# Performance work log

Measured on AMD Instinct MI355X. Metric: run time of the kernel, lower is better.

The kernel has to match this reference:

```python
import jax, jax.numpy as jnp
import numpy as np

IN_FEATURES = 4096
OUT_FEATURES = 14336
TOPK_RATIO = 0.3
TOPK = int(IN_FEATURES * TOPK_RATIO)  # 1228


def setup_inputs() -> dict:
    key = jax.random.key(0)
    k1, k2, k3 = jax.random.split(key, 3)
    x = jax.random.normal(k1, (1, 1, IN_FEATURES), dtype=jnp.float32)
    weight = jax.random.normal(k2, (OUT_FEATURES, IN_FEATURES), dtype=jnp.float32)
    bias = jax.random.normal(k3, (OUT_FEATURES,), dtype=jnp.float32)
    return {"x": x, "weight": weight, "bias": bias}


def reference(x, weight, bias):
    # Decode path (bsz*seq == 1), first-call cache miss: indices come from
    # the current activation's top-k |x| values (recall==1.0 branch).
    bsz, seq, _ = x.shape
    xf = x.reshape(-1)  # [in_features]
    # argsort(|x|, descending)[:topk] == top_k on |x| (tie order irrelevant for the math)
    _, idx = jax.lax.top_k(jnp.abs(xf).astype(jnp.float32), TOPK)  # [topk]
    x_slice = xf[idx]                 # [topk]
    w_slice = weight[:, idx]          # [out_features, topk]
    # x[:, indices] @ weight_slice.T + bias
    out = jnp.einsum("k,ok->o", x_slice, w_slice) + bias  # [out_features]
    return out.reshape(bsz, seq, OUT_FEATURES)
```

## Files before the change

### kernel.cpp

```cpp
#include <hip/hip_runtime.h>
#include <hip/hip_bf16.h>

#define N_IN 4096
#define N_OUT 14336
#define TOPK 1228

__global__ __launch_bounds__(1024) void topk_mask_kernel(
    const float* __restrict__ x, float* __restrict__ x_masked) {
  __shared__ unsigned int s_abs[N_IN];
  __shared__ unsigned int s_hist[256];
  __shared__ unsigned int s_pk[4];
  __shared__ unsigned long long s_cmask[N_IN / 64];
  __shared__ unsigned int s_cbase[N_IN / 64];

  const int tid = threadIdx.x;
  const int lane = tid & 63;

#pragma unroll
  for (int it = 0; it < N_IN / 1024; ++it) {
    const int i = it * 1024 + tid;
    s_abs[i] = __float_as_uint(x[i]) & 0x7fffffffu;
  }
  if (tid == 0) { s_pk[0] = 0u; s_pk[1] = TOPK; }
  __syncthreads();

  for (int pass = 3; pass >= 0; --pass) {
    const unsigned int prefix = s_pk[0];
    const unsigned int krem = s_pk[1];
    if (tid < 256) s_hist[tid] = 0u;
    __syncthreads();

    const int shift = pass * 8;
    const unsigned int maskAbove =
        (pass == 3) ? 0u : (0xFFFFFFFFu << (shift + 8));

#pragma unroll
    for (int it = 0; it < N_IN / 1024; ++it) {
      const int i = it * 1024 + tid;
      const unsigned int b = s_abs[i];
      const bool active = ((b & maskAbove) == prefix);
      const unsigned int bucket = (b >> shift) & 0xFFu;
      unsigned long long m = __ballot(active);
#pragma unroll
      for (int bit = 0; bit < 8; ++bit) {
        const unsigned long long vote =
            __ballot(active && ((bucket >> bit) & 1u));
        m &= ((bucket >> bit) & 1u) ? vote : ~vote;
      }
      if (active) {
        const int leader = __ffsll((unsigned long long)m) - 1;
        if (lane == leader)
          atomicAdd(&s_hist[bucket], (unsigned int)__popcll(m));
      }
    }
    __syncthreads();

    if (tid < 64) {
      const unsigned int h0 = s_hist[tid * 4 + 0];
      const unsigned int h1 = s_hist[tid * 4 + 1];
      const unsigned int h2 = s_hist[tid * 4 + 2];
      const unsigned int h3 = s_hist[tid * 4 + 3];
      const unsigned int s = h0 + h1 + h2 + h3;
      unsigned int inc = s;
#pragma unroll
      for (int off = 1; off < 64; off <<= 1) {
        const unsigned int v = __shfl_down(inc, off, 64);
        if (tid + off < 64) inc += v;
      }
      const unsigned int U = inc - s;
      const unsigned int C3 = U + h3;
      const unsigned int C2 = C3 + h2;
      const unsigned int C1 = C2 + h1;
      const unsigned int C0 = C1 + h0;
      const unsigned int Carr[4] = {C0, C1, C2, C3};
      const unsigned int Sarr[4] = {C1, C2, C3, U};
      const unsigned int hv[4] = {h0, h1, h2, h3};
#pragma unroll
      for (int j = 0; j < 4; ++j) {
        if (Sarr[j] < krem && krem <= Carr[j]) {
          s_pk[0] = prefix | ((unsigned int)(tid * 4 + j) << shift);
          s_pk[1] = krem - Sarr[j];
          s_pk[2] = hv[j];
        }
      }
    }
    __syncthreads();
  }

  const unsigned int t_abs = s_pk[0];
  const unsigned int need = s_pk[1];
  const unsigned int eqc = s_pk[2];

  if (eqc == need) {
#pragma unroll
    for (int it = 0; it < N_IN / 1024; ++it) {
      const int i = it * 1024 + tid;
      x_masked[i] = (s_abs[i] >= t_abs) ? x[i] : 0.0f;
    }
  } else {
#pragma unroll
    for (int it = 0; it < N_IN / 1024; ++it) {
      const int i = it * 1024 + tid;
      const bool eq = (s_abs[i] == t_abs);
      const unsigned long long m = __ballot(eq);
      if (lane == 0) s_cmask[i >> 6] = m;
    }
    __syncthreads();
    if (tid < 64) {
      const unsigned int cnt = (unsigned int)__popcll(s_cmask[tid]);
      unsigned int inc = cnt;
#pragma unroll
      for (int off = 1; off < 64; off <<= 1) {
        const unsigned int v = __shfl_up(inc, off, 64);
        if (lane >= off) inc += v;
      }
      s_cbase[tid] = inc - cnt;
    }
    __syncthreads();
#pragma unroll
    for (int it = 0; it < N_IN / 1024; ++it) {
      const int i = it * 1024 + tid;
      const unsigned int b = s_abs[i];
      bool sel = (b > t_abs);
      if (b == t_abs) {
        const unsigned long long below =
            s_cmask[i >> 6] & ((1ull << lane) - 1ull);
        sel = (s_cbase[i >> 6] + (unsigned int)__popcll(below)) < need;
      }
      x_masked[i] = sel ? x[i] : 0.0f;
    }
  }
}

__global__ __launch_bounds__(256) void masked_matvec_kernel(
    const float* __restrict__ xm, const float* __restrict__ W,
    const float* __restrict__ bias, float* __restrict__ out) {
  __shared__ __align__(16) float s_x[N_IN];

  const int tid = threadIdx.x;
  for (int i = tid; i < N_IN; i += 256) s_x[i] = xm[i];
  __syncthreads();

  const int wave = tid >> 6;
  const int lane = tid & 63;
  const int row = blockIdx.x * 4 + wave;
  const float4* __restrict__ wr4 =
      reinterpret_cast<const float4*>(W + (size_t)row * N_IN);
  const float4* s_x4 = reinterpret_cast<const float4*>(s_x);

  float a0 = 0.0f, a1 = 0.0f, a2 = 0.0f, a3 = 0.0f;
#pragma unroll
  for (int it = 0; it < 4; ++it) {
    const int b = it * 4 * 64 + lane;
    const float4 w0 = wr4[b + 0 * 64];
    const float4 w1 = wr4[b + 1 * 64];
    const float4 w2 = wr4[b + 2 * 64];
    const float4 w3 = wr4[b + 3 * 64];
    const float4 v0 = s_x4[b + 0 * 64];
    const float4 v1 = s_x4[b + 1 * 64];
    const float4 v2 = s_x4[b + 2 * 64];
    const float4 v3 = s_x4[b + 3 * 64];
    a0 += w0.x * v0.x + w0.y * v0.y + w0.z * v0.z + w0.w * v0.w;
    a1 += w1.x * v1.x + w1.y * v1.y + w1.z * v1.z + w1.w * v1.w;
    a2 += w2.x * v2.x + w2.y * v2.y + w2.z * v2.z + w2.w * v2.w;
    a3 += w3.x * v3.x + w3.y * v3.y + w3.z * v3.z + w3.w * v3.w;
  }
  float acc = (a0 + a1) + (a2 + a3);

#pragma unroll
  for (int off = 32; off >= 1; off >>= 1) acc += __shfl_down(acc, off, 64);

  if (lane == 0) out[row] = acc + bias[row];
}

extern "C" void kernel_launch(void* const* d_in, const int* in_sizes, int n_in,
                              void* d_out, int out_size, void* d_ws,
                              size_t ws_size, hipStream_t stream) {
  const float* x    = (const float*)d_in[0];
  const float* W    = (const float*)d_in[1];
  const float* bias = (const float*)d_in[2];
  float* out = (float*)d_out;
  float* xm  = (float*)d_ws;

  topk_mask_kernel<<<1, 1024, 0, stream>>>(x, xm);
  masked_matvec_kernel<<<N_OUT / 4, 256, 0, stream>>>(xm, W, bias, out);
}
```

Measured before the change: 54.84 us.

## Process two rows per wave, read x from global, stagger column phase

The matvec kernel now has each wave compute two output rows, so each block covers 8 rows. It drops the LDS staging of x and keeps the whole x slice for each lane in registers, loaded straight from global memory (L2-cached). Column chunks are visited in a rotating order offset per row pair, which spreads concurrent loads across memory channels. The cost is heavier register use (16 float4 of x plus weight prefetch), which may lower occupancy on a kernel bound by memory bandwidth.

```diff
diff --git a/kernel.cpp b/kernel.cpp
--- a/kernel.cpp
+++ b/kernel.cpp
@@ -135,42 +135,67 @@
 __global__ __launch_bounds__(256) void masked_matvec_kernel(
     const float* __restrict__ xm, const float* __restrict__ W,
     const float* __restrict__ bias, float* __restrict__ out) {
-  __shared__ __align__(16) float s_x[N_IN];
-
   const int tid = threadIdx.x;
-  for (int i = tid; i < N_IN; i += 256) s_x[i] = xm[i];
-  __syncthreads();
-
   const int wave = tid >> 6;
   const int lane = tid & 63;
-  const int row = blockIdx.x * 4 + wave;
-  const float4* __restrict__ wr4 =
-      reinterpret_cast<const float4*>(W + (size_t)row * N_IN);
-  const float4* s_x4 = reinterpret_cast<const float4*>(s_x);
-
-  float a0 = 0.0f, a1 = 0.0f, a2 = 0.0f, a3 = 0.0f;
-#pragma unroll
-  for (int it = 0; it < 4; ++it) {
-    const int b = it * 4 * 64 + lane;
-    const float4 w0 = wr4[b + 0 * 64];
-    const float4 w1 = wr4[b + 1 * 64];
-    const float4 w2 = wr4[b + 2 * 64];
-    const float4 w3 = wr4[b + 3 * 64];
-    const float4 v0 = s_x4[b + 0 * 64];
-    const float4 v1 = s_x4[b + 1 * 64];
-    const float4 v2 = s_x4[b + 2 * 64];
-    const float4 v3 = s_x4[b + 3 * 64];
-    a0 += w0.x * v0.x + w0.y * v0.y + w0.z * v0.z + w0.w * v0.w;
-    a1 += w1.x * v1.x + w1.y * v1.y + w1.z * v1.z + w1.w * v1.w;
-    a2 += w2.x * v2.x + w2.y * v2.y + w2.z * v2.z + w2.w * v2.w;
-    a3 += w3.x * v3.x + w3.y * v3.y + w3.z * v3.z + w3.w * v3.w;
-  }
-  float acc = (a0 + a1) + (a2 + a3);
-
-#pragma unroll
-  for (int off = 32; off >= 1; off >>= 1) acc += __shfl_down(acc, off, 64);
-
-  if (lane == 0) out[row] = acc + bias[row];
+  const int r0 = blockIdx.x * 8 + wave * 2;
+  const int phase = (r0 >> 1) & 15;
+
+  const float4* __restrict__ w0r4 =
+      reinterpret_cast<const float4*>(W + (size_t)r0 * N_IN);
+  const float4* __restrict__ w1r4 =
+      reinterpret_cast<const float4*>(W + (size_t)(r0 + 1) * N_IN);
+  const float4* __restrict__ x4 = reinterpret_cast<const float4*>(xm);
+
+  float4 p0[4], p1[4];
+#pragma unroll
+  for (int j = 0; j < 4; ++j) {
+    const int c = (phase + j) & 15;
+    p0[j] = w0r4[c * 64 + lane];
+    p1[j] = w1r4[c * 64 + lane];
+  }
+
+  float4 xv[16];
+#pragma unroll
+  for (int j = 0; j < 16; ++j) {
+    const int c = (phase + j) & 15;
+    xv[j] = x4[c * 64 + lane];
+  }
+
+  float a0[4], a1[4];
+#pragma unroll
+  for (int j = 0; j < 4; ++j) {
+    a0[j] = p0[j].x * xv[j].x + p0[j].y * xv[j].y + p0[j].z * xv[j].z +
+            p0[j].w * xv[j].w;
+    a1[j] = p1[j].x * xv[j].x + p1[j].y * xv[j].y + p1[j].z * xv[j].z +
+            p1[j].w * xv[j].w;
+  }
+
+#pragma unroll
+  for (int g = 1; g < 4; ++g) {
+#pragma unroll
+    for (int j = 0; j < 4; ++j) {
+      const int c = (phase + g * 4 + j) & 15;
+      const float4 u0 = w0r4[c * 64 + lane];
+      const float4 u1 = w1r4[c * 64 + lane];
+      const float4 v = xv[g * 4 + j];
+      a0[j] += u0.x * v.x + u0.y * v.y + u0.z * v.z + u0.w * v.w;
+      a1[j] += u1.x * v.x + u1.y * v.y + u1.z * v.z + u1.w * v.w;
+    }
+  }
+  float acc0 = (a0[0] + a0[1]) + (a0[2] + a0[3]);
+  float acc1 = (a1[0] + a1[1]) + (a1[2] + a1[3]);
+
+#pragma unroll
+  for (int off = 32; off >= 1; off >>= 1) {
+    acc0 += __shfl_down(acc0, off, 64);
+    acc1 += __shfl_down(acc1, off, 64);
+  }
+
+  if (lane == 0) {
+    out[r0] = acc0 + bias[r0];
+    out[r0 + 1] = acc1 + bias[r0 + 1];
+  }
 }
 
 extern "C" void kernel_launch(void* const* d_in, const int* in_sizes, int n_in,
@@ -183,5 +208,5 @@
   float* xm  = (float*)d_ws;
 
   topk_mask_kernel<<<1, 1024, 0, stream>>>(x, xm);
-  masked_matvec_kernel<<<N_OUT / 4, 256, 0, stream>>>(xm, W, bias, out);
+  masked_matvec_kernel<<<N_OUT / 8, 256, 0, stream>>>(xm, W, bias, out);
 }
```

Measured after the change: 51.51 us. -6.1%, faster.

## Restructure matvec: 8 rows per block, x in registers, nontemporal weight loads

Applied to the files above, without the earlier changes.

The masked matvec now assigns 8 weight rows per 256-thread block. Each thread keeps its fixed slice of x in registers instead of staging x through LDS, and streams a contiguous 8-row slab of W. Partial sums are reduced across the wave and then across the four waves through a small shared array. Weight loads use nontemporal hints to avoid polluting cache. The aim is to drop the per-block LDS fill of x and make weight streaming more contiguous, at the cost of more accumulator registers and an extra cross-wave reduction.

```diff
diff --git a/kernel.cpp b/kernel.cpp
--- a/kernel.cpp
+++ b/kernel.cpp
@@ -4,6 +4,8 @@
 #define N_IN 4096
 #define N_OUT 14336
 #define TOPK 1228
+
+typedef float f32x4 __attribute__((ext_vector_type(4)));
 
 __global__ __launch_bounds__(1024) void topk_mask_kernel(
     const float* __restrict__ x, float* __restrict__ x_masked) {
@@ -135,42 +137,49 @@
 __global__ __launch_bounds__(256) void masked_matvec_kernel(
     const float* __restrict__ xm, const float* __restrict__ W,
     const float* __restrict__ bias, float* __restrict__ out) {
-  __shared__ __align__(16) float s_x[N_IN];
+  __shared__ float s_part[4][8];
 
   const int tid = threadIdx.x;
-  for (int i = tid; i < N_IN; i += 256) s_x[i] = xm[i];
+  const int wave = tid >> 6;
+  const int lane = tid & 63;
+  const int row0 = blockIdx.x * 8;
+
+  const f32x4* __restrict__ slab4 =
+      reinterpret_cast<const f32x4*>(W + (size_t)row0 * N_IN);
+  const f32x4* __restrict__ x4 = reinterpret_cast<const f32x4*>(xm);
+
+  f32x4 xv[4];
+#pragma unroll
+  for (int j = 0; j < 4; ++j) xv[j] = x4[j * 256 + tid];
+
+  float acc[8];
+#pragma unroll
+  for (int r = 0; r < 8; ++r) acc[r] = 0.0f;
+
+#pragma unroll
+  for (int it = 0; it < 32; ++it) {
+    const f32x4 w = __builtin_nontemporal_load(&slab4[it * 256 + tid]);
+    const f32x4 v = xv[it & 3];
+    acc[it >> 2] += w.x * v.x + w.y * v.y + w.z * v.z + w.w * v.w;
+  }
+
+#pragma unroll
+  for (int r = 0; r < 8; ++r) {
+#pragma unroll
+    for (int off = 32; off >= 1; off >>= 1)
+      acc[r] += __shfl_down(acc[r], off, 64);
+  }
+  if (lane == 0) {
+#pragma unroll
+    for (int r = 0; r < 8; ++r) s_part[wave][r] = acc[r];
+  }
   __syncthreads();
 
-  const int wave = tid >> 6;
-  const int lane = tid & 63;
-  const int row = blockIdx.x * 4 + wave;
-  const float4* __restrict__ wr4 =
-      reinterpret_cast<const float4*>(W + (size_t)row * N_IN);
-  const float4* s_x4 = reinterpret_cast<const float4*>(s_x);
-
-  float a0 = 0.0f, a1 = 0.0f, a2 = 0.0f, a3 = 0.0f;
-#pragma unroll
-  for (int it = 0; it < 4; ++it) {
-    const int b = it * 4 * 64 + lane;
-    const float4 w0 = wr4[b + 0 * 64];
-    const float4 w1 = wr4[b + 1 * 64];
-    const float4 w2 = wr4[b + 2 * 64];
-    const float4 w3 = wr4[b + 3 * 64];
-    const float4 v0 = s_x4[b + 0 * 64];
-    const float4 v1 = s_x4[b + 1 * 64];
-    const float4 v2 = s_x4[b + 2 * 64];
-    const float4 v3 = s_x4[b + 3 * 64];
-    a0 += w0.x * v0.x + w0.y * v0.y + w0.z * v0.z + w0.w * v0.w;
-    a1 += w1.x * v1.x + w1.y * v1.y + w1.z * v1.z + w1.w * v1.w;
-    a2 += w2.x * v2.x + w2.y * v2.y + w2.z * v2.z + w2.w * v2.w;
-    a3 += w3.x * v3.x + w3.y * v3.y + w3.z * v3.z + w3.w * v3.w;
+  if (tid < 8) {
+    const float sum =
+        s_part[0][tid] + s_part[1][tid] + s_part[2][tid] + s_part[3][tid];
+    out[row0 + tid] = sum + bias[row0 + tid];
   }
-  float acc = (a0 + a1) + (a2 + a3);
-
-#pragma unroll
-  for (int off = 32; off >= 1; off >>= 1) acc += __shfl_down(acc, off, 64);
-
-  if (lane == 0) out[row] = acc + bias[row];
 }
 
 extern "C" void kernel_launch(void* const* d_in, const int* in_sizes, int n_in,
@@ -183,5 +192,5 @@
   float* xm  = (float*)d_ws;
 
   topk_mask_kernel<<<1, 1024, 0, stream>>>(x, xm);
-  masked_matvec_kernel<<<N_OUT / 4, 256, 0, stream>>>(xm, W, bias, out);
+  masked_matvec_kernel<<<N_OUT / 8, 256, 0, stream>>>(xm, W, bias, out);
 }
```

Result: faster. 51.36 us (-6.3%).
